# Kernel optimization log

Measured on AMD Instinct MI355X. Metric: run time of the kernel, lower is better.

## Reference

```python
import jax, jax.numpy as jnp
import numpy as np

B, N, D, H = 32, 8192, 128, 128


def setup_inputs() -> dict:
    key = jax.random.key(0)
    ks = jax.random.split(key, 9)
    s = lambda k, shp, fan: jax.random.normal(k, shp, jnp.float32) / np.sqrt(fan)
    return {
        "x": jax.random.normal(ks[0], (B, N, D), jnp.float32),
        "Wg1": s(ks[1], (D, H), D), "bg1": jnp.zeros((H,), jnp.float32),
        "Wg2": s(ks[2], (H, 1), H), "bg2": jnp.zeros((1,), jnp.float32),
        "Wn1": s(ks[3], (D, H), D), "bn1": jnp.zeros((H,), jnp.float32),
        "Wn2": s(ks[4], (H, H), H), "bn2": jnp.zeros((H,), jnp.float32),
    }


def reference(x, Wg1, bg1, Wg2, bg2, Wn1, bn1, Wn2, bn2):
    # gate_nn: Linear -> SiLU -> Linear(->1); scores per node
    gate = jnp.einsum("bnd,dh->bnh", x, Wg1) + bg1
    gate = jax.nn.silu(gate)
    gate = jnp.einsum("bnh,ho->bno", gate, Wg2) + bg2  # [B,N,1]
    # nn: Linear -> SiLU -> Linear; transformed node features
    h = jax.nn.silu(jnp.einsum("bnd,dh->bnh", x, Wn1) + bn1)
    h = jnp.einsum("bnh,hk->bnk", h, Wn2) + bn2  # [B,N,H]
    # segment softmax over nodes of each graph (segments == batch dim here)
    attn = jax.nn.softmax(gate, axis=1)  # [B,N,1]
    # weighted-sum pooling per graph
    return jnp.sum(attn * h, axis=1)  # [B,H]
```

## Files before the change

kernel.cpp:

```cpp
#include <hip/hip_runtime.h>

#define B_ 32
#define N_ 8192
#define D_ 128
#define H_ 128
#define R_ (B_ * N_)

#define NBLK 4096

typedef _Float16 f16;
typedef __attribute__((ext_vector_type(4))) _Float16 f16x4;
typedef __attribute__((ext_vector_type(8))) _Float16 f16x8;
typedef __attribute__((ext_vector_type(4))) float f32x4;

static constexpr size_t WPACK_OFF = 0;
static constexpr size_t VPART_OFF = 98304;
static constexpr size_t SPART_OFF = VPART_OFF + (size_t)NBLK * 128 * 4;

__device__ __forceinline__ float silu_f(float v) {
    return v * __builtin_amdgcn_rcpf(1.0f + __expf(-v));
}

__device__ __forceinline__ f32x4 mfma16(f16x8 a, f16x8 b, f32x4 c) {
    return __builtin_amdgcn_mfma_f32_16x16x32_f16(a, b, c, 0, 0, 0);
}

__global__ void k0_prepack(const float* __restrict__ Wg1,
                           const float* __restrict__ Wn1,
                           const float* __restrict__ Wn2,
                           f16* __restrict__ wp) {
    int tid = blockIdx.x * 256 + threadIdx.x;
    int m    = tid >> 14;
    int r    = tid & 16383;
    int j    = r & 7;
    int lane = (r >> 3) & 63;
    int kc   = (r >> 9) & 3;
    int nt   = r >> 11;
    int k = kc * 32 + (lane >> 4) * 8 + j;
    int n = nt * 16 + (lane & 15);
    const float* W = (m == 0) ? Wg1 : (m == 1) ? Wn1 : Wn2;
    wp[tid] = (f16)W[k * 128 + n];
}

__global__ __launch_bounds__(256, 3) void k1_fused(
        const float* __restrict__ x,
        const float* __restrict__ bg1, const float* __restrict__ wg2,
        const float* __restrict__ bg2, const float* __restrict__ bn1,
        const f16* __restrict__ wp,
        float* __restrict__ vpart, float* __restrict__ spart) {
    __shared__ f16 xlds[64 * 128];
    __shared__ f16 h1lds[64 * 128];
    __shared__ float gpart[4][64];

    const int tid  = threadIdx.x;
    const int w    = tid >> 6;
    const int lane = tid & 63;
    const int q    = lane >> 4;
    const int c    = lane & 15;

    const long rowbase = (long)blockIdx.x * 64;
    const float4* xg = (const float4*)x + rowbase * 32;
    float4 xv[8];
#pragma unroll
    for (int s = 0; s < 8; ++s) xv[s] = xg[s * 256 + tid];

    const f16x8* wpv = (const f16x8*)wp;
    f16x8 fg1[2][4], fn1[2][4];
#pragma unroll
    for (int s = 0; s < 2; ++s)
#pragma unroll
        for (int kc = 0; kc < 4; ++kc) {
            int base = ((2 * w + s) * 4 + kc) * 64 + lane;
            fg1[s][kc] = wpv[base];
            fn1[s][kc] = wpv[2048 + base];
        }
    float bg1q[2][4], wg2q[2][4], bn1q[2][4];
#pragma unroll
    for (int s = 0; s < 2; ++s)
#pragma unroll
        for (int r = 0; r < 4; ++r) {
            int col = (2 * w + s) * 16 + q * 4 + r;
            bg1q[s][r] = bg1[col];
            wg2q[s][r] = wg2[col];
            bn1q[s][r] = bn1[col];
        }
    const float bg2v = bg2[0];

    const int loh_e = (q * 16 + (c ^ q)) * 8;
    const int loh_o = (q * 16 + (c ^ (q | 4))) * 8;
    int h1wb[2];
#pragma unroll
    for (int s = 0; s < 2; ++s) {
        int q2 = s * 2 + (q >> 1);
        int v2 = ((w & 1) << 2) | q2;
        h1wb[s] = w * 512 + (q2 * 16 + (c ^ v2)) * 8 + (q & 1) * 4;
    }

#pragma unroll
    for (int s = 0; s < 8; ++s) {
        int e   = s * 256 + tid;
        int row = e >> 5, c4 = e & 31;
        int mt = row >> 4, cc = row & 15;
        int kc = c4 >> 3, qq = (c4 >> 1) & 3, j = (c4 & 1) * 4;
        int sw = (c4 >> 1) & 7;
        float4 vv = xv[s];
        f16x4 hv = {(f16)vv.x, (f16)vv.y, (f16)vv.z, (f16)vv.w};
        *(f16x4*)&xlds[((mt * 4 + kc) * 64 + qq * 16 + (cc ^ sw)) * 8 + j] = hv;
    }
    __syncthreads();

#pragma unroll
    for (int mt = 0; mt < 4; ++mt) {
        f16x8 a[4];
#pragma unroll
        for (int kc = 0; kc < 4; ++kc)
            a[kc] = *(const f16x8*)&xlds[(mt * 4 + kc) * 512 +
                                         ((kc & 1) ? loh_o : loh_e)];
        f32x4 ag[2] = {{0.f,0.f,0.f,0.f},{0.f,0.f,0.f,0.f}};
        f32x4 an[2] = {{0.f,0.f,0.f,0.f},{0.f,0.f,0.f,0.f}};
#pragma unroll
        for (int kc = 0; kc < 4; ++kc) {
#pragma unroll
            for (int s = 0; s < 2; ++s) {
                ag[s] = mfma16(fg1[s][kc], a[kc], ag[s]);
                an[s] = mfma16(fn1[s][kc], a[kc], an[s]);
            }
        }
#pragma unroll
        for (int s = 0; s < 2; ++s) {
            f16x4 h4;
#pragma unroll
            for (int r = 0; r < 4; ++r) h4[r] = (f16)silu_f(an[s][r] + bn1q[s][r]);
            *(f16x4*)&h1lds[mt * 2048 + h1wb[s]] = h4;
        }
        float p = 0.f;
#pragma unroll
        for (int s = 0; s < 2; ++s)
#pragma unroll
            for (int r = 0; r < 4; ++r)
                p += silu_f(ag[s][r] + bg1q[s][r]) * wg2q[s][r];
        p += __shfl_xor(p, 16);
        p += __shfl_xor(p, 32);
        if (lane < 16) gpart[w][mt * 16 + lane] = p;
    }

    f16x8 fn2[2][4];
#pragma unroll
    for (int s = 0; s < 2; ++s)
#pragma unroll
        for (int kc = 0; kc < 4; ++kc)
            fn2[s][kc] = wpv[4096 + ((2 * w + s) * 4 + kc) * 64 + lane];

    __syncthreads();

    float e4[4];
#pragma unroll
    for (int mt = 0; mt < 4; ++mt) {
        float g = bg2v + gpart[0][mt * 16 + c] + gpart[1][mt * 16 + c]
                       + gpart[2][mt * 16 + c] + gpart[3][mt * 16 + c];
        e4[mt] = __expf(g);
    }

    float V[2][4] = {{0.f,0.f,0.f,0.f},{0.f,0.f,0.f,0.f}};
#pragma unroll
    for (int mt = 0; mt < 4; ++mt) {
        f16x8 b[4];
#pragma unroll
        for (int kc = 0; kc < 4; ++kc)
            b[kc] = *(const f16x8*)&h1lds[(mt * 4 + kc) * 512 +
                                          ((kc & 1) ? loh_o : loh_e)];
        f32x4 acc[2] = {{0.f,0.f,0.f,0.f},{0.f,0.f,0.f,0.f}};
#pragma unroll
        for (int kc = 0; kc < 4; ++kc)
#pragma unroll
            for (int s = 0; s < 2; ++s)
                acc[s] = mfma16(fn2[s][kc], b[kc], acc[s]);
#pragma unroll
        for (int s = 0; s < 2; ++s)
#pragma unroll
            for (int r = 0; r < 4; ++r) V[s][r] += e4[mt] * acc[s][r];
    }

#pragma unroll
    for (int m = 1; m < 16; m <<= 1)
#pragma unroll
        for (int s = 0; s < 2; ++s)
#pragma unroll
            for (int r = 0; r < 4; ++r) V[s][r] += __shfl_xor(V[s][r], m);
    if (c == 0) {
#pragma unroll
        for (int s = 0; s < 2; ++s) {
            float4 o = {V[s][0], V[s][1], V[s][2], V[s][3]};
            *(float4*)&vpart[(long)blockIdx.x * 128 + (2 * w + s) * 16 + q * 4] = o;
        }
    }
    if (w == 0) {
        float Sl = e4[0] + e4[1] + e4[2] + e4[3];
#pragma unroll
        for (int m = 1; m < 16; m <<= 1) Sl += __shfl_xor(Sl, m);
        if (lane == 0) spart[blockIdx.x] = Sl;
    }
}

__global__ void k2_combine(const float* __restrict__ vpart,
                           const float* __restrict__ spart,
                           const float* __restrict__ bn2,
                           float* __restrict__ out) {
    const int b = blockIdx.x;
    const int t = threadIdx.x;
    const int j = t & 127;
    const int half = t >> 7;

    const float* vp = vpart + (long)b * 128 * 128;
    float v = 0.f;
#pragma unroll
    for (int k = 0; k < 64; ++k)
        v += vp[(half * 64 + k) * 128 + j];

    __shared__ float vred[128];
    __shared__ float sred[4];
    if (half == 0) vred[j] = v;

    float s = (t < 128) ? spart[b * 128 + t] : 0.f;
#pragma unroll
    for (int m = 1; m < 64; m <<= 1) s += __shfl_xor(s, m);
    if (t < 128 && (t & 63) == 0) sred[t >> 6] = s;
    __syncthreads();
    if (half == 1) vred[j] += v;
    __syncthreads();
    if (t < 128) {
        float denom = sred[0] + sred[1];
        out[b * 128 + t] = vred[t] / denom + bn2[t];
    }
}

extern "C" void kernel_launch(void* const* d_in, const int* in_sizes, int n_in,
                              void* d_out, int out_size, void* d_ws, size_t ws_size,
                              hipStream_t stream) {
    const float* x   = (const float*)d_in[0];
    const float* Wg1 = (const float*)d_in[1];
    const float* bg1 = (const float*)d_in[2];
    const float* Wg2 = (const float*)d_in[3];
    const float* bg2 = (const float*)d_in[4];
    const float* Wn1 = (const float*)d_in[5];
    const float* bn1 = (const float*)d_in[6];
    const float* Wn2 = (const float*)d_in[7];
    const float* bn2 = (const float*)d_in[8];
    float* out = (float*)d_out;

    char* ws = (char*)d_ws;
    f16*   wp    = (f16*)(ws + WPACK_OFF);
    float* vpart = (float*)(ws + VPART_OFF);
    float* spart = (float*)(ws + SPART_OFF);

    k0_prepack<<<192, 256, 0, stream>>>(Wg1, Wn1, Wn2, wp);
    k1_fused<<<NBLK, 256, 0, stream>>>(x, bg1, Wg2, bg2, bn1, wp, vpart, spart);
    k2_combine<<<32, 256, 0, stream>>>(vpart, spart, bn2, out);
}
```

Baseline: 213.0 us.

## Hoist second linear layer past softmax pooling and process two tiles per block

Uses linearity to pool the SiLU hidden activations weighted by the softmax numerators first, then applies Wn2 once per graph in the combine kernel. This removes the per-row second GEMM, the h1 LDS staging and the Wn2 fragment loads from the main kernel. Each block now handles two 64-row tiles, prefetching the next tile's x into registers while the current one is computed, which halves the partial-sum traffic. The pooled accumulation now uses fp16-rounded hidden values in scalar FMAs, and the small 128x128 matvec in the combine kernel runs serially per output column.

```diff
diff --git a/kernel.cpp b/kernel.cpp
--- a/kernel.cpp
+++ b/kernel.cpp
@@ -6,7 +6,8 @@
 #define H_ 128
 #define R_ (B_ * N_)
 
-#define NBLK 4096
+#define TILES 2
+#define NBLK1 2048
 
 typedef _Float16 f16;
 typedef __attribute__((ext_vector_type(4))) _Float16 f16x4;
@@ -14,8 +15,8 @@
 typedef __attribute__((ext_vector_type(4))) float f32x4;
 
 static constexpr size_t WPACK_OFF = 0;
-static constexpr size_t VPART_OFF = 98304;
-static constexpr size_t SPART_OFF = VPART_OFF + (size_t)NBLK * 128 * 4;
+static constexpr size_t VPART_OFF = 65536;
+static constexpr size_t SPART_OFF = VPART_OFF + (size_t)NBLK1 * 128 * 4;
 
 __device__ __forceinline__ float silu_f(float v) {
     return v * __builtin_amdgcn_rcpf(1.0f + __expf(-v));
@@ -27,7 +28,6 @@
 
 __global__ void k0_prepack(const float* __restrict__ Wg1,
                            const float* __restrict__ Wn1,
-                           const float* __restrict__ Wn2,
                            f16* __restrict__ wp) {
     int tid = blockIdx.x * 256 + threadIdx.x;
     int m    = tid >> 14;
@@ -38,7 +38,7 @@
     int nt   = r >> 11;
     int k = kc * 32 + (lane >> 4) * 8 + j;
     int n = nt * 16 + (lane & 15);
-    const float* W = (m == 0) ? Wg1 : (m == 1) ? Wn1 : Wn2;
+    const float* W = m ? Wn1 : Wg1;
     wp[tid] = (f16)W[k * 128 + n];
 }
 
@@ -49,7 +49,6 @@
         const f16* __restrict__ wp,
         float* __restrict__ vpart, float* __restrict__ spart) {
     __shared__ f16 xlds[64 * 128];
-    __shared__ f16 h1lds[64 * 128];
     __shared__ float gpart[4][64];
 
     const int tid  = threadIdx.x;
@@ -58,7 +57,7 @@
     const int q    = lane >> 4;
     const int c    = lane & 15;
 
-    const long rowbase = (long)blockIdx.x * 64;
+    const long rowbase = (long)blockIdx.x * (64 * TILES);
     const float4* xg = (const float4*)x + rowbase * 32;
     float4 xv[8];
 #pragma unroll
@@ -88,97 +87,79 @@
 
     const int loh_e = (q * 16 + (c ^ q)) * 8;
     const int loh_o = (q * 16 + (c ^ (q | 4))) * 8;
-    int h1wb[2];
-#pragma unroll
-    for (int s = 0; s < 2; ++s) {
-        int q2 = s * 2 + (q >> 1);
-        int v2 = ((w & 1) << 2) | q2;
-        h1wb[s] = w * 512 + (q2 * 16 + (c ^ v2)) * 8 + (q & 1) * 4;
-    }
-
-#pragma unroll
-    for (int s = 0; s < 8; ++s) {
-        int e   = s * 256 + tid;
-        int row = e >> 5, c4 = e & 31;
-        int mt = row >> 4, cc = row & 15;
-        int kc = c4 >> 3, qq = (c4 >> 1) & 3, j = (c4 & 1) * 4;
-        int sw = (c4 >> 1) & 7;
-        float4 vv = xv[s];
-        f16x4 hv = {(f16)vv.x, (f16)vv.y, (f16)vv.z, (f16)vv.w};
-        *(f16x4*)&xlds[((mt * 4 + kc) * 64 + qq * 16 + (cc ^ sw)) * 8 + j] = hv;
-    }
-    __syncthreads();
-
-#pragma unroll
-    for (int mt = 0; mt < 4; ++mt) {
-        f16x8 a[4];
-#pragma unroll
-        for (int kc = 0; kc < 4; ++kc)
-            a[kc] = *(const f16x8*)&xlds[(mt * 4 + kc) * 512 +
-                                         ((kc & 1) ? loh_o : loh_e)];
-        f32x4 ag[2] = {{0.f,0.f,0.f,0.f},{0.f,0.f,0.f,0.f}};
-        f32x4 an[2] = {{0.f,0.f,0.f,0.f},{0.f,0.f,0.f,0.f}};
-#pragma unroll
-        for (int kc = 0; kc < 4; ++kc) {
+
+    float V[2][4] = {{0.f, 0.f, 0.f, 0.f}, {0.f, 0.f, 0.f, 0.f}};
+    float Sacc = 0.f;
+
+#pragma unroll
+    for (int t = 0; t < TILES; ++t) {
+#pragma unroll
+        for (int s = 0; s < 8; ++s) {
+            int e   = s * 256 + tid;
+            int row = e >> 5, c4 = e & 31;
+            int mt = row >> 4, cc = row & 15;
+            int kc = c4 >> 3, qq = (c4 >> 1) & 3, j = (c4 & 1) * 4;
+            int sw = (c4 >> 1) & 7;
+            float4 vv = xv[s];
+            f16x4 hv = {(f16)vv.x, (f16)vv.y, (f16)vv.z, (f16)vv.w};
+            *(f16x4*)&xlds[((mt * 4 + kc) * 64 + qq * 16 + (cc ^ sw)) * 8 + j] = hv;
+        }
+        if (t + 1 < TILES) {
+#pragma unroll
+            for (int s = 0; s < 8; ++s)
+                xv[s] = xg[(t + 1) * 2048 + s * 256 + tid];
+        }
+        __syncthreads();
+
+        f16x4 hq[4][2];
+#pragma unroll
+        for (int mt = 0; mt < 4; ++mt) {
+            f16x8 a[4];
+#pragma unroll
+            for (int kc = 0; kc < 4; ++kc)
+                a[kc] = *(const f16x8*)&xlds[(mt * 4 + kc) * 512 +
+                                             ((kc & 1) ? loh_o : loh_e)];
+            f32x4 ag[2] = {{0.f,0.f,0.f,0.f},{0.f,0.f,0.f,0.f}};
+            f32x4 an[2] = {{0.f,0.f,0.f,0.f},{0.f,0.f,0.f,0.f}};
+#pragma unroll
+            for (int kc = 0; kc < 4; ++kc) {
+#pragma unroll
+                for (int s = 0; s < 2; ++s) {
+                    ag[s] = mfma16(fg1[s][kc], a[kc], ag[s]);
+                    an[s] = mfma16(fn1[s][kc], a[kc], an[s]);
+                }
+            }
 #pragma unroll
             for (int s = 0; s < 2; ++s) {
-                ag[s] = mfma16(fg1[s][kc], a[kc], ag[s]);
-                an[s] = mfma16(fn1[s][kc], a[kc], an[s]);
+                f16x4 h4;
+#pragma unroll
+                for (int r = 0; r < 4; ++r) h4[r] = (f16)silu_f(an[s][r] + bn1q[s][r]);
+                hq[mt][s] = h4;
             }
-        }
-#pragma unroll
-        for (int s = 0; s < 2; ++s) {
-            f16x4 h4;
-#pragma unroll
-            for (int r = 0; r < 4; ++r) h4[r] = (f16)silu_f(an[s][r] + bn1q[s][r]);
-            *(f16x4*)&h1lds[mt * 2048 + h1wb[s]] = h4;
-        }
-        float p = 0.f;
-#pragma unroll
-        for (int s = 0; s < 2; ++s)
-#pragma unroll
-            for (int r = 0; r < 4; ++r)
-                p += silu_f(ag[s][r] + bg1q[s][r]) * wg2q[s][r];
-        p += __shfl_xor(p, 16);
-        p += __shfl_xor(p, 32);
-        if (lane < 16) gpart[w][mt * 16 + lane] = p;
-    }
-
-    f16x8 fn2[2][4];
-#pragma unroll
-    for (int s = 0; s < 2; ++s)
-#pragma unroll
-        for (int kc = 0; kc < 4; ++kc)
-            fn2[s][kc] = wpv[4096 + ((2 * w + s) * 4 + kc) * 64 + lane];
-
-    __syncthreads();
-
-    float e4[4];
-#pragma unroll
-    for (int mt = 0; mt < 4; ++mt) {
-        float g = bg2v + gpart[0][mt * 16 + c] + gpart[1][mt * 16 + c]
-                       + gpart[2][mt * 16 + c] + gpart[3][mt * 16 + c];
-        e4[mt] = __expf(g);
-    }
-
-    float V[2][4] = {{0.f,0.f,0.f,0.f},{0.f,0.f,0.f,0.f}};
-#pragma unroll
-    for (int mt = 0; mt < 4; ++mt) {
-        f16x8 b[4];
-#pragma unroll
-        for (int kc = 0; kc < 4; ++kc)
-            b[kc] = *(const f16x8*)&h1lds[(mt * 4 + kc) * 512 +
-                                          ((kc & 1) ? loh_o : loh_e)];
-        f32x4 acc[2] = {{0.f,0.f,0.f,0.f},{0.f,0.f,0.f,0.f}};
-#pragma unroll
-        for (int kc = 0; kc < 4; ++kc)
+            float p = 0.f;
 #pragma unroll
             for (int s = 0; s < 2; ++s)
-                acc[s] = mfma16(fn2[s][kc], b[kc], acc[s]);
-#pragma unroll
-        for (int s = 0; s < 2; ++s)
-#pragma unroll
-            for (int r = 0; r < 4; ++r) V[s][r] += e4[mt] * acc[s][r];
+#pragma unroll
+                for (int r = 0; r < 4; ++r)
+                    p += silu_f(ag[s][r] + bg1q[s][r]) * wg2q[s][r];
+            p += __shfl_xor(p, 16);
+            p += __shfl_xor(p, 32);
+            if (lane < 16) gpart[w][mt * 16 + lane] = p;
+        }
+        __syncthreads();
+
+#pragma unroll
+        for (int mt = 0; mt < 4; ++mt) {
+            float g = bg2v + gpart[0][mt * 16 + c] + gpart[1][mt * 16 + c]
+                           + gpart[2][mt * 16 + c] + gpart[3][mt * 16 + c];
+            float e4 = __expf(g);
+            Sacc += e4;
+#pragma unroll
+            for (int s = 0; s < 2; ++s)
+#pragma unroll
+                for (int r = 0; r < 4; ++r)
+                    V[s][r] += e4 * (float)hq[mt][s][r];
+        }
     }
 
 #pragma unroll
@@ -195,42 +176,43 @@
         }
     }
     if (w == 0) {
-        float Sl = e4[0] + e4[1] + e4[2] + e4[3];
-#pragma unroll
-        for (int m = 1; m < 16; m <<= 1) Sl += __shfl_xor(Sl, m);
-        if (lane == 0) spart[blockIdx.x] = Sl;
+#pragma unroll
+        for (int m = 1; m < 16; m <<= 1) Sacc += __shfl_xor(Sacc, m);
+        if (lane == 0) spart[blockIdx.x] = Sacc;
     }
 }
 
 __global__ void k2_combine(const float* __restrict__ vpart,
                            const float* __restrict__ spart,
+                           const float* __restrict__ Wn2,
                            const float* __restrict__ bn2,
                            float* __restrict__ out) {
     const int b = blockIdx.x;
     const int t = threadIdx.x;
-    const int j = t & 127;
-    const int half = t >> 7;
-
-    const float* vp = vpart + (long)b * 128 * 128;
+
+    __shared__ float pooled[128];
+    __shared__ float sred;
+
     float v = 0.f;
-#pragma unroll
-    for (int k = 0; k < 64; ++k)
-        v += vp[(half * 64 + k) * 128 + j];
-
-    __shared__ float vred[128];
-    __shared__ float sred[4];
-    if (half == 0) vred[j] = v;
-
-    float s = (t < 128) ? spart[b * 128 + t] : 0.f;
+    if (t < 128) {
+        const float* vp = vpart + (long)b * 64 * 128;
+#pragma unroll 8
+        for (int k = 0; k < 64; ++k) v += vp[k * 128 + t];
+    }
+
+    float s = (t < 64) ? spart[b * 64 + t] : 0.f;
 #pragma unroll
     for (int m = 1; m < 64; m <<= 1) s += __shfl_xor(s, m);
-    if (t < 128 && (t & 63) == 0) sred[t >> 6] = s;
+    if (t == 0) sred = s;
+
     __syncthreads();
-    if (half == 1) vred[j] += v;
+    if (t < 128) pooled[t] = v / sred;
     __syncthreads();
     if (t < 128) {
-        float denom = sred[0] + sred[1];
-        out[b * 128 + t] = vred[t] / denom + bn2[t];
+        float acc = bn2[t];
+#pragma unroll 8
+        for (int k = 0; k < 128; ++k) acc += pooled[k] * Wn2[k * 128 + t];
+        out[b * 128 + t] = acc;
     }
 }
 
@@ -253,7 +235,7 @@
     float* vpart = (float*)(ws + VPART_OFF);
     float* spart = (float*)(ws + SPART_OFF);
 
-    k0_prepack<<<192, 256, 0, stream>>>(Wg1, Wn1, Wn2, wp);
-    k1_fused<<<NBLK, 256, 0, stream>>>(x, bg1, Wg2, bg2, bn1, wp, vpart, spart);
-    k2_combine<<<32, 256, 0, stream>>>(vpart, spart, bn2, out);
-}
+    k0_prepack<<<128, 256, 0, stream>>>(Wg1, Wn1, wp);
+    k1_fused<<<NBLK1, 256, 0, stream>>>(x, bg1, Wg2, bg2, bn1, wp, vpart, spart);
+    k2_combine<<<32, 256, 0, stream>>>(vpart, spart, Wn2, bn2, out);
+}
```

Measured after the change: 298.9 us. +40.3%, slower.
